# Kernel tuning notes

Hardware: AMD Instinct MI355X
Metric: run time of the kernel (lower is better)

## Reference

```python
import jax, jax.numpy as jnp
import numpy as np

DROPOUT_P = 0.1
EMBED = 128  # head dim; inv_scale_factor = sqrt(EMBED)


def setup_inputs() -> dict:
    key = jax.random.key(0)
    ks = jax.random.split(key, 9)
    B, S, H, D = 4, 2048, 16, EMBED
    mk = lambda k, shape: jax.random.normal(k, shape, dtype=jnp.float32)
    return {
        "query": mk(ks[0], (B, S, H, D)),
        "key": mk(ks[1], (B, S, H, D)),
        "value": mk(ks[2], (B, S, H, D)),
        "Wq": mk(ks[3], (D, D)) / np.sqrt(D),
        "bq": mk(ks[4], (D,)) * 0.01,
        "Wk": mk(ks[5], (D, D)) / np.sqrt(D),
        "bk": mk(ks[6], (D,)) * 0.01,
        "Wv": mk(ks[7], (D, D)) / np.sqrt(D),
        "bv": mk(ks[8], (D,)) * 0.01,
    }


def reference(query, key, value, Wq, bq, Wk, bk, Wv, bv):
    # Linear (torch convention: x @ W.T + b) then permute(0,2,1,3): [B,S,H,D] -> [B,H,S,D]
    q = (query @ Wq.T + bq).transpose(0, 2, 1, 3)
    k = (key @ Wk.T + bk).transpose(0, 2, 1, 3)
    v = (value @ Wv.T + bv).transpose(0, 2, 1, 3)
    scale = 1.0 / jnp.sqrt(jnp.float32(EMBED))  # div by embed_size**0.5
    scores = jnp.einsum("bhqd,bhkd->bhqk", q, k) * scale
    probs = jax.nn.softmax(scores, axis=-1)
    # deterministic inverted dropout with fixed key (train-mode dropout)
    keep = jax.random.bernoulli(jax.random.key(42), 1.0 - DROPOUT_P, probs.shape)
    probs = jnp.where(keep, probs / (1.0 - DROPOUT_P), 0.0)
    return jnp.einsum("bhqk,bhkd->bhqd", probs, v)
```

## Files before the change

### kernel.cpp

```cpp
#include <hip/hip_runtime.h>
#include <stdint.h>

#define BB 4
#define SS 2048
#define HH 16
#define DD 128

typedef __attribute__((ext_vector_type(8))) short bf16x8;
typedef __attribute__((ext_vector_type(4))) float f32x4;

__device__ __forceinline__ float bf2f(uint16_t u) {
  union { uint32_t i; float f; } x; x.i = ((uint32_t)u) << 16; return x.f;
}
__device__ __forceinline__ uint16_t f2bf(float f) {
  union { float f; uint32_t i; } u; u.f = f;
  uint32_t r = u.i + 0x7FFFu + ((u.i >> 16) & 1u);
  return (uint16_t)(r >> 16);
}

#define TF_C 3865470464u
#define TF_ROUND(r) { x0 += x1; x1 = __builtin_amdgcn_alignbit(x1, x1, 32 - (r)) ^ x0; }

__device__ __forceinline__ void tf2x32(uint32_t k0, uint32_t k1, uint32_t c0, uint32_t c1,
                                       uint32_t& o0, uint32_t& o1) {
  const uint32_t k2 = 0x1BD11BDAu ^ k0 ^ k1;
  uint32_t x0 = c0 + k0, x1 = c1 + k1;
  TF_ROUND(13) TF_ROUND(15) TF_ROUND(26) TF_ROUND(6)
  x0 += k1; x1 += k2 + 1u;
  TF_ROUND(17) TF_ROUND(29) TF_ROUND(16) TF_ROUND(24)
  x0 += k2; x1 += k0 + 2u;
  TF_ROUND(13) TF_ROUND(15) TF_ROUND(26) TF_ROUND(6)
  x0 += k0; x1 += k1 + 3u;
  TF_ROUND(17) TF_ROUND(29) TF_ROUND(16) TF_ROUND(24)
  x0 += k1; x1 += k2 + 4u;
  TF_ROUND(13) TF_ROUND(15) TF_ROUND(26) TF_ROUND(6)
  x0 += k2; x1 += k0 + 5u;
  o0 = x0; o1 = x1;
}

__device__ __forceinline__ uint32_t tf_bit_part(uint32_t i) {
  uint32_t o0, o1;
  tf2x32(0u, 42u, 0u, i, o0, o1);
  return ((o0 ^ o1) < TF_C) ? 1u : 0u;
}

__global__ void detect_kernel(const uint16_t* __restrict__ q, int* __restrict__ flag) {
  if (blockIdx.x == 0 && threadIdx.x == 0) {
    int ok = 1;
    for (int i = 0; i < 64; ++i) {
      float a = fabsf(bf2f(q[2 * i]));
      if (!(a == 0.0f || (a > 9.0e-13f && a < 64.0f))) ok = 0;
    }
    *flag = ok;
  }
}

__global__ __launch_bounds__(256, 3) void proj_kernel(
    const void* __restrict__ xq, const void* __restrict__ xk, const void* __restrict__ xv,
    const void* __restrict__ Wq, const void* __restrict__ bq,
    const void* __restrict__ Wk, const void* __restrict__ bk,
    const void* __restrict__ Wv, const void* __restrict__ bv,
    uint16_t* __restrict__ Qo, uint16_t* __restrict__ Ko, uint16_t* __restrict__ Vo,
    const int* __restrict__ flag) {
  __shared__ __align__(16) uint16_t Wl[128 * 128];
  __shared__ __align__(16) char Tep[4][5120];
  const int isbf = *flag;
  const int tz = blockIdx.y;
  const void* x = (tz == 0) ? xq : (tz == 1) ? xk : xv;
  const void* W = (tz == 0) ? Wq : (tz == 1) ? Wk : Wv;
  const void* bs = (tz == 0) ? bq : (tz == 1) ? bk : bv;
  uint16_t* out = (tz == 0) ? Qo : (tz == 1) ? Ko : Vo;
  const int vtrans = (tz == 2);

  const int tid = threadIdx.x;
  const int wave = tid >> 6, lane = tid & 63;
  const int c = lane & 15, quad = lane >> 4;
  const int bh = blockIdx.x >> 5;
  const int s0 = (blockIdx.x & 31) * 64;
  const int sw = s0 + wave * 16;
  const int b = bh >> 4, h = bh & 15;

  {
    const int row = tid >> 1;
    const int cb = (tid & 1) * 8;
    char* wl = (char*)Wl + row * 256;
    if (isbf) {
      const uint16_t* wr = (const uint16_t*)W + (size_t)row * DD + (tid & 1) * 64;
#pragma unroll
      for (int i = 0; i < 8; ++i) {
        bf16x8 v = *(const bf16x8*)(wr + i * 8);
        *(bf16x8*)(wl + ((((cb + i) << 4)) ^ ((row & 7) << 4))) = v;
      }
    } else {
      const float* wr = (const float*)W + (size_t)row * DD + (tid & 1) * 64;
#pragma unroll
      for (int i = 0; i < 8; ++i) {
        bf16x8 v;
#pragma unroll
        for (int j = 0; j < 8; ++j) v[j] = (short)f2bf(wr[i * 8 + j]);
        *(bf16x8*)(wl + ((((cb + i) << 4)) ^ ((row & 7) << 4))) = v;
      }
    }
  }

  bf16x8 af[4];
  {
    const size_t xrow = ((size_t)(b * SS + sw + c) * HH + h) * DD;
    if (isbf) {
      const uint16_t* xr = (const uint16_t*)x + xrow + quad * 8;
#pragma unroll
      for (int t = 0; t < 4; ++t) af[t] = *(const bf16x8*)(xr + t * 32);
    } else {
      const float* xr = (const float*)x + xrow + quad * 8;
#pragma unroll
      for (int t = 0; t < 4; ++t) {
#pragma unroll
        for (int j = 0; j < 8; ++j) af[t][j] = (short)f2bf(xr[t * 32 + j]);
      }
    }
  }
  __syncthreads();

  char* myT = Tep[wave];
  uint16_t* tq = (uint16_t*)myT;

  for (int nt = 0; nt < 8; ++nt) {
    f32x4 acc = {0.f, 0.f, 0.f, 0.f};
    const int n = nt * 16 + c;
    const char* wb = (char*)Wl + n * 256;
    const int nsw = (c & 7) << 4;
#pragma unroll
    for (int t = 0; t < 4; ++t) {
      bf16x8 wf = *(const bf16x8*)(wb + (((quad + t * 4) << 4) ^ nsw));
      acc = __builtin_amdgcn_mfma_f32_16x16x32_bf16(af[t], wf, acc, 0, 0, 0);
    }
    const float bias = isbf ? bf2f(((const uint16_t*)bs)[n]) : ((const float*)bs)[n];
    if (!vtrans) {
#pragma unroll
      for (int r = 0; r < 4; ++r)
        tq[(quad * 4 + r) * 136 + n] = f2bf(acc[r] + bias);
    } else {
      uint32_t p01 = (uint32_t)f2bf(acc[0] + bias) | ((uint32_t)f2bf(acc[1] + bias) << 16);
      uint32_t p23 = (uint32_t)f2bf(acc[2] + bias) | ((uint32_t)f2bf(acc[3] + bias) << 16);
      *(uint64_t*)(myT + n * 40 + quad * 8) = (uint64_t)p01 | ((uint64_t)p23 << 32);
    }
  }

  if (!vtrans) {
    const size_t rb = (size_t)(bh * SS + sw + c) * DD;
#pragma unroll
    for (int p = 0; p < 4; ++p) {
      const int ch = quad + 4 * p;
      bf16x8 v = *(const bf16x8*)(myT + c * 272 + ch * 16);
      *(bf16x8*)(out + rb + ch * 8) = v;
    }
  } else {
    const size_t vb = (size_t)bh * (SS * DD);
#pragma unroll
    for (int p = 0; p < 4; ++p) {
      const int d = p * 32 + (lane >> 1), oct = lane & 1;
      bf16x8 v = *(const bf16x8*)(myT + d * 40 + oct * 16);
      const int sg = s0 + wave * 16 + oct * 8;
      *(bf16x8*)(out + vb + (size_t)(sg >> 5) * 4096 + d * 32 + (sg & 31)) = v;
    }
  }
}

__global__ __launch_bounds__(256, 4) void attn_kernel(
    const uint16_t* __restrict__ Q, const uint16_t* __restrict__ K, const uint16_t* __restrict__ Vt,
    void* __restrict__ outv, const int* __restrict__ flag) {
  __shared__ __align__(16) uint16_t Ks[2][32][128];
  __shared__ __align__(16) uint16_t Vs[2][128][32];
  __shared__ __align__(16) uint16_t pl[4][16][40];
  const int isbf = *flag;
  const int tid = threadIdx.x;
  const int wave = tid >> 6, lane = tid & 63;
  const int c = lane & 15, quad = lane >> 4;
  const int bh = blockIdx.x >> 5;
  const int q0 = (blockIdx.x & 31) * 64 + wave * 16;

  const uint16_t* Qb = Q + (size_t)bh * SS * DD;
  const uint16_t* Kb = K + (size_t)bh * SS * DD;
  const uint16_t* Vb = Vt + (size_t)bh * SS * DD;

  bf16x8 qf[4];
  {
    const uint16_t* qr = Qb + (q0 + c) * DD + quad * 8;
#pragma unroll
    for (int t = 0; t < 4; ++t) qf[t] = *(const bf16x8*)(qr + t * 32);
  }

  const f32x4 zero = {0.f, 0.f, 0.f, 0.f};
  f32x4 o[8];
#pragma unroll
  for (int i = 0; i < 8; ++i) o[i] = zero;
  float lsum[4] = {0.f, 0.f, 0.f, 0.f};

  const float sc2 = 0.12751744f;

  uint32_t ibase[4];
#pragma unroll
  for (int r = 0; r < 4; ++r)
    ibase[r] = ((uint32_t)bh * SS + (uint32_t)(q0 + quad * 4 + r)) * SS + (uint32_t)c;

  uint16_t(*plw)[40] = pl[wave];

  const int krow = tid >> 4;
  const int kd0 = krow * 256 + (((tid & 15) * 16) ^ ((krow & 7) << 4));
  const int kd1 = kd0 + 16 * 256;
  const int vswz = ((tid >> 3) & 3) << 4;
  const int vd0 = (tid * 16) ^ vswz, vd1 = vd0 + 4096;
  const uint16_t* kga = Kb + krow * DD + (tid & 15) * 8;
  const uint16_t* vga = Vb + tid * 8;

  bf16x8 ksa = *(const bf16x8*)(kga);
  bf16x8 ksb = *(const bf16x8*)(kga + 16 * DD);
  bf16x8 vsa = *(const bf16x8*)(vga);
  bf16x8 vsb = *(const bf16x8*)(vga + 2048);
  {
    char* kd = (char*)Ks[0]; *(bf16x8*)(kd + kd0) = ksa; *(bf16x8*)(kd + kd1) = ksb;
    char* vd = (char*)Vs[0]; *(bf16x8*)(vd + vd0) = vsa; *(bf16x8*)(vd + vd1) = vsb;
  }
  __syncthreads();

  const int ksw = (c & 7) << 4;
  const int vr0 = (c * 64 + quad * 16) ^ ((((c >> 1) & 3)) << 4);
  int cur = 0;

  for (int kt = 0; kt < SS / 32; ++kt) {
    const int ktn = (kt + 1) & 63;
    ksa = *(const bf16x8*)(kga + ktn * 32 * DD);
    ksb = *(const bf16x8*)(kga + ktn * 32 * DD + 16 * DD);
    vsa = *(const bf16x8*)(vga + ktn * 4096);
    vsb = *(const bf16x8*)(vga + ktn * 4096 + 2048);

    const char* klds = (const char*)Ks[cur];
    f32x4 sf[2];
#pragma unroll
    for (int ks = 0; ks < 2; ++ks) {
      f32x4 acc = zero;
      const char* kr = klds + (ks * 16 + c) * 256;
#pragma unroll
      for (int t = 0; t < 4; ++t) {
        bf16x8 kf = *(const bf16x8*)(kr + ((quad * 16 + t * 64) ^ ksw));
        acc = __builtin_amdgcn_mfma_f32_16x16x32_bf16(qf[t], kf, acc, 0, 0, 0);
      }
      sf[ks] = acc;
    }
    const uint32_t ik = (uint32_t)kt * 32u;
#pragma unroll
    for (int ks = 0; ks < 2; ++ks) {
#pragma unroll
      for (int r = 0; r < 4; ++r) {
        float p = __builtin_amdgcn_exp2f(sf[ks][r] * sc2);
        lsum[r] += p;
        uint32_t b0, b1;
        tf2x32(0u, 42u, 0u, ibase[r] + ik + (uint32_t)(ks * 16), b0, b1);
        float pm = ((b0 ^ b1) < TF_C) ? p : 0.0f;
        plw[quad * 4 + r][ks * 16 + c] = f2bf(pm);
      }
    }
    bf16x8 pa = *(const bf16x8*)(&plw[c][quad * 8]);
    const char* vlds = (const char*)Vs[cur] + vr0;
#pragma unroll
    for (int dt = 0; dt < 8; ++dt) {
      bf16x8 vf = *(const bf16x8*)(vlds + dt * 1024);
      o[dt] = __builtin_amdgcn_mfma_f32_16x16x32_bf16(pa, vf, o[dt], 0, 0, 0);
    }

    {
      char* kd = (char*)Ks[cur ^ 1]; *(bf16x8*)(kd + kd0) = ksa; *(bf16x8*)(kd + kd1) = ksb;
      char* vd = (char*)Vs[cur ^ 1]; *(bf16x8*)(vd + vd0) = vsa; *(bf16x8*)(vd + vd1) = vsb;
    }
    __syncthreads();
    cur ^= 1;
  }

#pragma unroll
  for (int r = 0; r < 4; ++r) {
    float v = lsum[r];
    v += __shfl_xor(v, 1);
    v += __shfl_xor(v, 2);
    v += __shfl_xor(v, 4);
    v += __shfl_xor(v, 8);
    lsum[r] = 1.0f / (0.9f * v);
  }

  const size_t ob = (size_t)bh * SS * DD;
  if (isbf) {
    uint16_t* outp = (uint16_t*)outv;
#pragma unroll
    for (int dt = 0; dt < 8; ++dt)
#pragma unroll
      for (int r = 0; r < 4; ++r)
        outp[ob + (size_t)(q0 + quad * 4 + r) * DD + dt * 16 + c] = f2bf(o[dt][r] * lsum[r]);
  } else {
    float* outp = (float*)outv;
#pragma unroll
    for (int dt = 0; dt < 8; ++dt)
#pragma unroll
      for (int r = 0; r < 4; ++r)
        outp[ob + (size_t)(q0 + quad * 4 + r) * DD + dt * 16 + c] = o[dt][r] * lsum[r];
  }

  if (blockIdx.x == 0 && wave == 0) {
    uint32_t o0, o1;
    tf2x32(0u, 0u, 0u, 0u, o0, o1);
    bool bad1 = (o0 != 0x6b200159u) || (o1 != 0x99ba4efeu);
#pragma unroll
    for (int ks = 0; ks < 2; ++ks)
#pragma unroll
      for (int r = 0; r < 4; ++r)
        plw[quad * 4 + r][ks * 16 + c] = f2bf((float)((quad * 4 + r) * 32 + ks * 16 + c));
    bf16x8 tp = *(const bf16x8*)(&plw[c][quad * 8]);
    bool bad3 = false;
#pragma unroll
    for (int j = 0; j < 8; ++j)
      bad3 |= ((uint16_t)tp[j] != f2bf((float)(c * 32 + quad * 8 + j)));
    bf16x8 ta, tb;
#pragma unroll
    for (int j = 0; j < 8; ++j) {
      ta[j] = (short)f2bf((float)(c * 32 + quad * 8 + j));
      tb[j] = (short)((quad * 8 + j == c) ? f2bf(1.0f) : 0);
    }
    f32x4 tc = zero;
    tc = __builtin_amdgcn_mfma_f32_16x16x32_bf16(ta, tb, tc, 0, 0, 0);
    bool bad4 = false;
#pragma unroll
    for (int r = 0; r < 4; ++r)
      bad4 |= (tc[r] != bf2f(f2bf((float)((quad * 4 + r) * 32 + c))));
#pragma unroll
    for (int j = 0; j < 8; ++j) {
      ta[j] = (short)((quad * 8 + j == c) ? f2bf(1.0f) : 0);
      tb[j] = (short)f2bf((float)(c * 32 + quad * 8 + j));
    }
    f32x4 td = zero;
    td = __builtin_amdgcn_mfma_f32_16x16x32_bf16(ta, tb, td, 0, 0, 0);
    bool bad5 = false;
#pragma unroll
    for (int r = 0; r < 4; ++r)
      bad5 |= (td[r] != bf2f(f2bf((float)(c * 32 + quad * 4 + r))));
    float main_d0 = __shfl(o[0][0] * lsum[0], 0);
    float main_d64 = __shfl(o[4][0] * lsum[0], 0);
    float a0 = 0.f, a64 = 0.f, al = 0.f;
    for (int k = lane; k < SS; k += 64) {
      float s = 0.f;
      for (int d = 0; d < DD; ++d) s += bf2f(Qb[d]) * bf2f(Kb[k * DD + d]);
      float p = __builtin_amdgcn_exp2f(s * sc2);
      al += p;
      if (tf_bit_part((uint32_t)k)) {
        a0 += p * bf2f(Vb[(size_t)(k >> 5) * 4096 + (k & 31)]);
        a64 += p * bf2f(Vb[(size_t)(k >> 5) * 4096 + 64 * 32 + (k & 31)]);
      }
    }
#pragma unroll
    for (int off = 32; off; off >>= 1) {
      a0 += __shfl_xor(a0, off);
      a64 += __shfl_xor(a64, off);
      al += __shfl_xor(al, off);
    }
    bool bad6 = (fabsf(a0 / (0.9f * al) - main_d0) > 0.02f) ||
                (fabsf(a64 / (0.9f * al) - main_d64) > 0.02f);

    unsigned long long m1 = __ballot(bad1), m3 = __ballot(bad3),
                       m4 = __ballot(bad4), m5 = __ballot(bad5), m6 = __ballot(bad6);
    if (lane == 0) {
      float s = 0.f;
      if (m1) s = 1e8f;
      else if (m3) s = 1e6f;
      else if (m4) s = 1e5f;
      else if (m5) s = 4e4f;
      else if (m6) s = 2e4f;
      if (s != 0.f) {
        if (isbf) ((uint16_t*)outv)[0] = f2bf(s);
        else ((float*)outv)[0] = s;
      }
    }
  }
}

extern "C" void kernel_launch(void* const* d_in, const int* in_sizes, int n_in,
                              void* d_out, int out_size, void* d_ws, size_t ws_size,
                              hipStream_t stream) {
  char* ws = (char*)d_ws;
  int* flag = (int*)ws;
  uint16_t* Qo = (uint16_t*)(ws + 256);
  uint16_t* Ko = Qo + (size_t)BB * HH * SS * DD;
  uint16_t* Vo = Ko + (size_t)BB * HH * SS * DD;

  hipLaunchKernelGGL(detect_kernel, dim3(1), dim3(64), 0, stream,
                     (const uint16_t*)d_in[0], flag);
  hipLaunchKernelGGL(proj_kernel, dim3(2048, 3), dim3(256), 0, stream,
                     d_in[0], d_in[1], d_in[2], d_in[3], d_in[4], d_in[5], d_in[6], d_in[7], d_in[8],
                     Qo, Ko, Vo, flag);
  hipLaunchKernelGGL(attn_kernel, dim3(2048), dim3(256), 0, stream,
                     Qo, Ko, Vo, d_out, flag);
}
```

Before: 972.6 us.

## Transpose QK MFMA and pass probabilities via ds_bpermute instead of LDS

```diff
diff --git a/kernel.cpp b/kernel.cpp
--- a/kernel.cpp
+++ b/kernel.cpp
@@ -16,6 +16,11 @@
   union { float f; uint32_t i; } u; u.f = f;
   uint32_t r = u.i + 0x7FFFu + ((u.i >> 16) & 1u);
   return (uint16_t)(r >> 16);
+}
+__device__ __forceinline__ uint32_t cvtpk_bf16(float lo, float hi) {
+  uint32_t d;
+  asm("v_cvt_pk_bf16_f32 %0, %1, %2" : "=v"(d) : "v"(lo), "v"(hi));
+  return d;
 }
 
 #define TF_C 3865470464u
@@ -171,7 +176,6 @@
     void* __restrict__ outv, const int* __restrict__ flag) {
   __shared__ __align__(16) uint16_t Ks[2][32][128];
   __shared__ __align__(16) uint16_t Vs[2][128][32];
-  __shared__ __align__(16) uint16_t pl[4][16][40];
   const int isbf = *flag;
   const int tid = threadIdx.x;
   const int wave = tid >> 6, lane = tid & 63;
@@ -194,16 +198,15 @@
   f32x4 o[8];
 #pragma unroll
   for (int i = 0; i < 8; ++i) o[i] = zero;
-  float lsum[4] = {0.f, 0.f, 0.f, 0.f};
+  float lsum = 0.f;
 
   const float sc2 = 0.12751744f;
 
-  uint32_t ibase[4];
-#pragma unroll
-  for (int r = 0; r < 4; ++r)
-    ibase[r] = ((uint32_t)bh * SS + (uint32_t)(q0 + quad * 4 + r)) * SS + (uint32_t)c;
-
-  uint16_t(*plw)[40] = pl[wave];
+  const uint32_t ibase = ((uint32_t)bh * SS + (uint32_t)(q0 + c)) * SS + (uint32_t)(quad * 4);
+
+  const int addrA = (c + 16 * ((quad & 1) << 1)) * 4;
+  const int addrB = addrA + 64;
+  const int hi2 = quad >> 1;
 
   const int krow = tid >> 4;
   const int kd0 = krow * 256 + (((tid & 15) * 16) ^ ((krow & 7) << 4));
@@ -234,6 +237,16 @@
     vsa = *(const bf16x8*)(vga + ktn * 4096);
     vsb = *(const bf16x8*)(vga + ktn * 4096 + 2048);
 
+    float fm[8];
+#pragma unroll
+    for (int ks = 0; ks < 2; ++ks)
+#pragma unroll
+      for (int r = 0; r < 4; ++r) {
+        uint32_t b0, b1;
+        tf2x32(0u, 42u, 0u, ibase + (uint32_t)(kt * 32 + ks * 16 + r), b0, b1);
+        fm[ks * 4 + r] = ((b0 ^ b1) < TF_C) ? 1.0f : 0.0f;
+      }
+
     const char* klds = (const char*)Ks[cur];
     f32x4 sf[2];
 #pragma unroll
@@ -243,29 +256,40 @@
 #pragma unroll
       for (int t = 0; t < 4; ++t) {
         bf16x8 kf = *(const bf16x8*)(kr + ((quad * 16 + t * 64) ^ ksw));
-        acc = __builtin_amdgcn_mfma_f32_16x16x32_bf16(qf[t], kf, acc, 0, 0, 0);
+        acc = __builtin_amdgcn_mfma_f32_16x16x32_bf16(kf, qf[t], acc, 0, 0, 0);
       }
       sf[ks] = acc;
     }
-    const uint32_t ik = (uint32_t)kt * 32u;
-#pragma unroll
-    for (int ks = 0; ks < 2; ++ks) {
+
+    float pm[2][4];
+#pragma unroll
+    for (int ks = 0; ks < 2; ++ks)
 #pragma unroll
       for (int r = 0; r < 4; ++r) {
         float p = __builtin_amdgcn_exp2f(sf[ks][r] * sc2);
-        lsum[r] += p;
-        uint32_t b0, b1;
-        tf2x32(0u, 42u, 0u, ibase[r] + ik + (uint32_t)(ks * 16), b0, b1);
-        float pm = ((b0 ^ b1) < TF_C) ? p : 0.0f;
-        plw[quad * 4 + r][ks * 16 + c] = f2bf(pm);
-      }
-    }
-    bf16x8 pa = *(const bf16x8*)(&plw[c][quad * 8]);
+        lsum += p;
+        pm[ks][r] = p * fm[ks * 4 + r];
+      }
+    uint32_t pk0[2], pk1[2];
+#pragma unroll
+    for (int rp = 0; rp < 2; ++rp) {
+      pk0[rp] = cvtpk_bf16(pm[0][2 * rp], pm[0][2 * rp + 1]);
+      pk1[rp] = cvtpk_bf16(pm[1][2 * rp], pm[1][2 * rp + 1]);
+    }
+    union { uint32_t u[4]; bf16x8 v; } pa;
+#pragma unroll
+    for (int t = 0; t < 4; ++t) {
+      const int a = (t < 2) ? addrA : addrB;
+      int lo = __builtin_amdgcn_ds_bpermute(a, (int)pk0[t & 1]);
+      int hi = __builtin_amdgcn_ds_bpermute(a, (int)pk1[t & 1]);
+      pa.u[t] = (uint32_t)(hi2 ? hi : lo);
+    }
+
     const char* vlds = (const char*)Vs[cur] + vr0;
 #pragma unroll
     for (int dt = 0; dt < 8; ++dt) {
       bf16x8 vf = *(const bf16x8*)(vlds + dt * 1024);
-      o[dt] = __builtin_amdgcn_mfma_f32_16x16x32_bf16(pa, vf, o[dt], 0, 0, 0);
+      o[dt] = __builtin_amdgcn_mfma_f32_16x16x32_bf16(pa.v, vf, o[dt], 0, 0, 0);
     }
 
     {
@@ -276,15 +300,12 @@
     cur ^= 1;
   }
 
-#pragma unroll
-  for (int r = 0; r < 4; ++r) {
-    float v = lsum[r];
-    v += __shfl_xor(v, 1);
-    v += __shfl_xor(v, 2);
-    v += __shfl_xor(v, 4);
-    v += __shfl_xor(v, 8);
-    lsum[r] = 1.0f / (0.9f * v);
-  }
+  lsum += __shfl_xor(lsum, 16);
+  lsum += __shfl_xor(lsum, 32);
+  const float linv = 1.0f / (0.9f * lsum);
+  float rinv[4];
+#pragma unroll
+  for (int r = 0; r < 4; ++r) rinv[r] = __shfl(linv, quad * 4 + r);
 
   const size_t ob = (size_t)bh * SS * DD;
   if (isbf) {
@@ -293,30 +314,46 @@
     for (int dt = 0; dt < 8; ++dt)
 #pragma unroll
       for (int r = 0; r < 4; ++r)
-        outp[ob + (size_t)(q0 + quad * 4 + r) * DD + dt * 16 + c] = f2bf(o[dt][r] * lsum[r]);
+        outp[ob + (size_t)(q0 + quad * 4 + r) * DD + dt * 16 + c] = f2bf(o[dt][r] * rinv[r]);
   } else {
     float* outp = (float*)outv;
 #pragma unroll
     for (int dt = 0; dt < 8; ++dt)
 #pragma unroll
       for (int r = 0; r < 4; ++r)
-        outp[ob + (size_t)(q0 + quad * 4 + r) * DD + dt * 16 + c] = o[dt][r] * lsum[r];
+        outp[ob + (size_t)(q0 + quad * 4 + r) * DD + dt * 16 + c] = o[dt][r] * rinv[r];
   }
 
   if (blockIdx.x == 0 && wave == 0) {
     uint32_t o0, o1;
     tf2x32(0u, 0u, 0u, 0u, o0, o1);
     bool bad1 = (o0 != 0x6b200159u) || (o1 != 0x99ba4efeu);
-#pragma unroll
-    for (int ks = 0; ks < 2; ++ks)
-#pragma unroll
-      for (int r = 0; r < 4; ++r)
-        plw[quad * 4 + r][ks * 16 + c] = f2bf((float)((quad * 4 + r) * 32 + ks * 16 + c));
-    bf16x8 tp = *(const bf16x8*)(&plw[c][quad * 8]);
     bool bad3 = false;
-#pragma unroll
-    for (int j = 0; j < 8; ++j)
-      bad3 |= ((uint16_t)tp[j] != f2bf((float)(c * 32 + quad * 8 + j)));
+    {
+      uint32_t tk0[2], tk1[2], tq0[2], tq1[2];
+#pragma unroll
+      for (int rp = 0; rp < 2; ++rp) {
+        tk0[rp] = cvtpk_bf16((float)(quad * 4 + 2 * rp), (float)(quad * 4 + 2 * rp + 1));
+        tk1[rp] = cvtpk_bf16((float)(16 + quad * 4 + 2 * rp), (float)(16 + quad * 4 + 2 * rp + 1));
+        tq0[rp] = cvtpk_bf16((float)c, (float)c);
+        tq1[rp] = tq0[rp];
+      }
+#pragma unroll
+      for (int t = 0; t < 4; ++t) {
+        const int a = (t < 2) ? addrA : addrB;
+        int lo = __builtin_amdgcn_ds_bpermute(a, (int)tk0[t & 1]);
+        int hi = __builtin_amdgcn_ds_bpermute(a, (int)tk1[t & 1]);
+        uint32_t wk = (uint32_t)(hi2 ? hi : lo);
+        uint32_t ek = (uint32_t)f2bf((float)(quad * 8 + 2 * t)) |
+                      ((uint32_t)f2bf((float)(quad * 8 + 2 * t + 1)) << 16);
+        bad3 |= (wk != ek);
+        lo = __builtin_amdgcn_ds_bpermute(a, (int)tq0[t & 1]);
+        hi = __builtin_amdgcn_ds_bpermute(a, (int)tq1[t & 1]);
+        uint32_t wq = (uint32_t)(hi2 ? hi : lo);
+        uint32_t eq = (uint32_t)f2bf((float)c) | ((uint32_t)f2bf((float)c) << 16);
+        bad3 |= (wq != eq);
+      }
+    }
     bf16x8 ta, tb;
 #pragma unroll
     for (int j = 0; j < 8; ++j) {
@@ -340,8 +377,8 @@
 #pragma unroll
     for (int r = 0; r < 4; ++r)
       bad5 |= (td[r] != bf2f(f2bf((float)(c * 32 + quad * 4 + r))));
-    float main_d0 = __shfl(o[0][0] * lsum[0], 0);
-    float main_d64 = __shfl(o[4][0] * lsum[0], 0);
+    float main_d0 = __shfl(o[0][0] * rinv[0], 0);
+    float main_d64 = __shfl(o[4][0] * rinv[0], 0);
     float a0 = 0.f, a64 = 0.f, al = 0.f;
     for (int k = lane; k < SS; k += 64) {
       float s = 0.f;
```

New measurement: 975.0 us. Within noise of the previous version (+0.3%).
